# Optimization experiments

Measured on AMD Instinct MI355X. Metric: run time of the kernel, lower is better.

## Reference

```python
import jax, jax.numpy as jnp
import numpy as np

N_NODES = 50000
N_EDGES = 800000
NUM_FEATURES = 128
H1, H2, H3 = 256, 512, 256


def setup_inputs() -> dict:
    key = jax.random.key(0)
    ks = jax.random.split(key, 14)

    def lin(kw, fan_in, fan_out):
        # torch nn.Linear-style init, stored as [in, out] for x @ W
        bound = 1.0 / np.sqrt(fan_in)
        W = jax.random.uniform(kw, (fan_in, fan_out), jnp.float32, -bound, bound)
        b = jnp.zeros((fan_out,), jnp.float32)
        return W, b

    x = jax.random.normal(ks[0], (N_NODES, NUM_FEATURES), jnp.float32)
    edge_index = jax.random.randint(ks[1], (2, N_EDGES), 0, N_NODES, jnp.int64 if jax.config.jax_enable_x64 else jnp.int32)

    W1, b1 = lin(ks[2], NUM_FEATURES, H1)
    W2, b2 = lin(ks[3], H1, H2)
    W3, b3 = lin(ks[4], H2, H3)
    Wf1, bf1 = lin(ks[5], H3, 128)
    Wf2, bf2 = lin(ks[6], 128, 64)
    Wf3, bf3 = lin(ks[7], 64, 1)

    return {"x": x, "edge_index": edge_index,
            "W1": W1, "b1": b1, "W2": W2, "b2": b2, "W3": W3, "b3": b3,
            "Wf1": Wf1, "bf1": bf1, "Wf2": Wf2, "bf2": bf2, "Wf3": Wf3, "bf3": bf3}


def gcn_conv(x, W, b, row, col, dinv_row_col, n):
    # PyG GCNConv: out = D^{-1/2} (A+I) D^{-1/2} (x W) + b, self-loops already in row/col
    h = x @ W                              # [N, out]
    msg = h[row] * dinv_row_col[:, None]   # gather + edge-wise scale: [E+N, out]
    return jax.ops.segment_sum(msg, col, num_segments=n) + b


def reference(x, edge_index, W1, b1, W2, b2, W3, b3, Wf1, bf1, Wf2, bf2, Wf3, bf3):
    n = x.shape[0]
    loop = jnp.arange(n, dtype=edge_index.dtype)
    row = jnp.concatenate([edge_index[0], loop])   # sources (with self-loops)
    col = jnp.concatenate([edge_index[1], loop])   # targets (with self-loops)

    # symmetric normalization (computed once; identical for all three convs)
    deg = jax.ops.segment_sum(jnp.ones(col.shape[0], x.dtype), col, num_segments=n)
    dinv = jnp.where(deg > 0, jax.lax.rsqrt(deg), 0.0)
    norm = dinv[row] * dinv[col]                   # [E+N]

    h = jax.nn.relu(gcn_conv(x, W1, b1, row, col, norm, n))
    h = jax.nn.relu(gcn_conv(h, W2, b2, row, col, norm, n))
    h = jax.nn.relu(gcn_conv(h, W3, b3, row, col, norm, n))

    g = jnp.mean(h, axis=0, keepdims=True)         # [1, H3]
    g = jax.nn.relu(g @ Wf1 + bf1)
    g = jax.nn.relu(g @ Wf2 + bf2)
    return g @ Wf3 + bf3                           # [1, 1]
```

## Files before the change

### kernel.cpp

```cpp
#include <hip/hip_runtime.h>
#include <hip/hip_bf16.h>

#define N_NODES 50000
#define N_EDGES 800000
#define N_BUCKETS 64
#define M_PAD 50048
#define SCAN_NB 196

typedef short short8 __attribute__((ext_vector_type(8)));
typedef float floatx4 __attribute__((ext_vector_type(4)));
typedef float floatx2 __attribute__((ext_vector_type(2)));

__device__ __forceinline__ unsigned short f2bf(float f) {
    unsigned u = __float_as_uint(f);
    unsigned r = (u + 0x7fff + ((u >> 16) & 1)) >> 16;
    return (unsigned short)r;
}
__device__ __forceinline__ float bf2f(unsigned short h) {
    return __uint_as_float(((unsigned)h) << 16);
}
__device__ __forceinline__ void expand2(unsigned u, float& lo, float& hi) {
    lo = __uint_as_float(u << 16);
    hi = __uint_as_float(u & 0xffff0000u);
}

__device__ __forceinline__ unsigned pack4_fp8(float f0, float f1, float f2, float f3) {
    int v = __builtin_amdgcn_cvt_pk_fp8_f32(f0, f1, 0, false);
    v = __builtin_amdgcn_cvt_pk_fp8_f32(f2, f3, v, true);
    return (unsigned)v;
}
__device__ __forceinline__ void accum_fp8x4(float* a, unsigned u, float w) {
    floatx2 lo = __builtin_amdgcn_cvt_pk_f32_fp8((int)u, false);
    floatx2 hi = __builtin_amdgcn_cvt_pk_f32_fp8((int)u, true);
    a[0] += lo[0] * w; a[1] += lo[1] * w;
    a[2] += hi[0] * w; a[3] += hi[1] * w;
}
__device__ __forceinline__ void accum_fp8x2(float* a, unsigned u, float w) {
    floatx2 lo = __builtin_amdgcn_cvt_pk_f32_fp8((int)u, false);
    a[0] += lo[0] * w; a[1] += lo[1] * w;
}

__device__ __forceinline__ void gload16(const void* gp, void* lp) {
    __builtin_amdgcn_global_load_lds(
        (const __attribute__((address_space(1))) unsigned int*)gp,
        (__attribute__((address_space(3))) unsigned int*)lp,
        16, 0, 0);
}

__global__ void k_init(int* __restrict__ cnt, float* __restrict__ gb) {
    int i = blockIdx.x * blockDim.x + threadIdx.x;
    if (i < N_NODES) cnt[i] = 0;
    if (i < N_BUCKETS * 256) gb[i] = 0.0f;
}

__global__ void k_count(const int* __restrict__ col, int* __restrict__ cnt) {
    int e = blockIdx.x * blockDim.x + threadIdx.x;
    if (e < N_EDGES) atomicAdd(&cnt[col[e]], 1);
}

__global__ __launch_bounds__(256) void k_scanA(const int* __restrict__ cnt,
                                               int* __restrict__ bsum) {
    __shared__ int red[256];
    int t = threadIdx.x;
    int i = blockIdx.x * 256 + t;
    red[t] = (i < N_NODES) ? cnt[i] : 0;
    __syncthreads();
    for (int d = 128; d > 0; d >>= 1) {
        if (t < d) red[t] += red[t + d];
        __syncthreads();
    }
    if (t == 0) bsum[blockIdx.x] = red[0];
}

__global__ __launch_bounds__(256) void k_scanB(const int* __restrict__ bsum,
                                               int* __restrict__ bbase,
                                               int* __restrict__ off) {
    __shared__ int sc[256];
    int t = threadIdx.x;
    sc[t] = (t < SCAN_NB) ? bsum[t] : 0;
    __syncthreads();
    for (int d = 1; d < 256; d <<= 1) {
        int v = 0;
        if (t >= d) v = sc[t - d];
        __syncthreads();
        if (t >= d) sc[t] += v;
        __syncthreads();
    }
    if (t < SCAN_NB) bbase[t] = sc[t] - bsum[t];
    if (t == 0) off[N_NODES] = N_EDGES;
}

__global__ __launch_bounds__(256) void k_scanC(const int* __restrict__ cnt,
                                               const int* __restrict__ bbase,
                                               int* __restrict__ off,
                                               int* __restrict__ cursor,
                                               float* __restrict__ dinv) {
    __shared__ int sc[256];
    int t = threadIdx.x;
    int i = blockIdx.x * 256 + t;
    int c = (i < N_NODES) ? cnt[i] : 0;
    sc[t] = c;
    __syncthreads();
    for (int d = 1; d < 256; d <<= 1) {
        int v = 0;
        if (t >= d) v = sc[t - d];
        __syncthreads();
        if (t >= d) sc[t] += v;
        __syncthreads();
    }
    if (i < N_NODES) {
        int excl = sc[t] - c + bbase[blockIdx.x];
        off[i] = excl;
        cursor[i] = excl;
        dinv[i] = 1.0f / sqrtf((float)(c + 1));
    }
}

__global__ void k_fill(const int* __restrict__ row, const int* __restrict__ col,
                       const float* __restrict__ dinv, int* __restrict__ cursor,
                       int2* __restrict__ epack) {
    int e = blockIdx.x * blockDim.x + threadIdx.x;
    if (e >= N_EDGES) return;
    int v = col[e];
    int p = atomicAdd(&cursor[v], 1);
    int r = row[e];
    epack[p] = make_int2(r, __float_as_int(dinv[r]));
}

__global__ void k_prepW(const float* __restrict__ W,
                        unsigned short* __restrict__ Th,
                        unsigned short* __restrict__ Tl, int K, int N) {
    int idx = blockIdx.x * blockDim.x + threadIdx.x;
    if (idx >= K * N) return;
    int n = idx / K, k = idx - n * K;
    float v = W[(size_t)k * N + n];
    unsigned short h = f2bf(v);
    Th[idx] = h;
    Tl[idx] = f2bf(v - bf2f(h));
}

__global__ void k_prepX8(const float* __restrict__ x, unsigned char* __restrict__ xq) {
    int i = blockIdx.x * blockDim.x + threadIdx.x;
    if (i >= N_NODES * 32) return;
    const float* s = x + (size_t)i * 4;
    *(unsigned*)&xq[(size_t)i * 4] = pack4_fp8(s[0], s[1], s[2], s[3]);
}

template <int DIM, int POOL>
__global__ __launch_bounds__(256) void k_aggf(
    const unsigned char* __restrict__ xq, const int* __restrict__ off,
    const int2* __restrict__ epack, const float* __restrict__ dinv,
    const float* __restrict__ bias, unsigned short* __restrict__ outb,
    float* __restrict__ gb) {
    const int FPL = DIM / 64;
    __shared__ float gpart[256];
    if (POOL) {
        gpart[threadIdx.x] = 0.0f;
        __syncthreads();
    }
    int wv = threadIdx.x >> 6;
    int li = threadIdx.x & 63;
    int v = blockIdx.x * 4 + wv;
    int f = li * FPL;
    float dv = dinv[v];
    const unsigned char* __restrict__ xf = xq + f;
    float a0[FPL], a1[FPL], a2[FPL], a3[FPL];
#pragma unroll
    for (int i = 0; i < FPL; ++i) { a0[i] = 0.f; a1[i] = 0.f; a2[i] = 0.f; a3[i] = 0.f; }
    if (FPL == 4) {
        accum_fp8x4(a0, *(const unsigned*)&xf[(size_t)v * DIM], dv);
    } else {
        accum_fp8x2(a0, (unsigned)*(const unsigned short*)&xf[(size_t)v * DIM], dv);
    }
    int s = off[v], e = off[v + 1];
    int j = s;
    for (; j + 4 <= e; j += 4) {
        int2 p0 = epack[j + 0];
        int2 p1 = epack[j + 1];
        int2 p2 = epack[j + 2];
        int2 p3 = epack[j + 3];
        if (FPL == 4) {
            unsigned g0 = *(const unsigned*)&xf[(size_t)p0.x * DIM];
            unsigned g1 = *(const unsigned*)&xf[(size_t)p1.x * DIM];
            unsigned g2 = *(const unsigned*)&xf[(size_t)p2.x * DIM];
            unsigned g3 = *(const unsigned*)&xf[(size_t)p3.x * DIM];
            accum_fp8x4(a0, g0, __int_as_float(p0.y));
            accum_fp8x4(a1, g1, __int_as_float(p1.y));
            accum_fp8x4(a2, g2, __int_as_float(p2.y));
            accum_fp8x4(a3, g3, __int_as_float(p3.y));
        } else {
            unsigned g0 = *(const unsigned short*)&xf[(size_t)p0.x * DIM];
            unsigned g1 = *(const unsigned short*)&xf[(size_t)p1.x * DIM];
            unsigned g2 = *(const unsigned short*)&xf[(size_t)p2.x * DIM];
            unsigned g3 = *(const unsigned short*)&xf[(size_t)p3.x * DIM];
            accum_fp8x2(a0, g0, __int_as_float(p0.y));
            accum_fp8x2(a1, g1, __int_as_float(p1.y));
            accum_fp8x2(a2, g2, __int_as_float(p2.y));
            accum_fp8x2(a3, g3, __int_as_float(p3.y));
        }
    }
    for (; j < e; ++j) {
        int2 p = epack[j];
        if (FPL == 4) {
            accum_fp8x4(a0, *(const unsigned*)&xf[(size_t)p.x * DIM], __int_as_float(p.y));
        } else {
            accum_fp8x2(a0, (unsigned)*(const unsigned short*)&xf[(size_t)p.x * DIM],
                        __int_as_float(p.y));
        }
    }
    float acc[FPL];
#pragma unroll
    for (int i = 0; i < FPL; ++i)
        acc[i] = ((a0[i] + a1[i]) + (a2[i] + a3[i])) * dv;
    if (!POOL) {
        if (FPL == 4) {
            uint2 o;
            o.x = (unsigned)f2bf(acc[0]) | ((unsigned)f2bf(acc[1]) << 16);
            o.y = (unsigned)f2bf(acc[2]) | ((unsigned)f2bf(acc[3]) << 16);
            *(uint2*)&outb[(size_t)v * DIM + f] = o;
        } else {
            unsigned o = (unsigned)f2bf(acc[0]) | ((unsigned)f2bf(acc[1]) << 16);
            *(unsigned*)&outb[(size_t)v * DIM + f] = o;
        }
    } else {
#pragma unroll
        for (int i = 0; i < FPL; ++i) {
            float r = fmaxf(acc[i] + bias[f + i], 0.0f);
            atomicAdd(&gpart[f + i], r);
        }
        __syncthreads();
        atomicAdd(&gb[(blockIdx.x & (N_BUCKETS - 1)) * 256 + threadIdx.x],
                  gpart[threadIdx.x]);
    }
}

template <int BIAS, int RELU, int OUTFP8>
__global__ __launch_bounds__(256) void k_gemm_b(
    const unsigned short* __restrict__ A,
    const unsigned short* __restrict__ Bh, const unsigned short* __restrict__ Bl,
    const float* __restrict__ bias, void* __restrict__ Cout,
    int M, int K, int N) {
    __shared__ unsigned short smem[3 * 2 * 4096];
    unsigned short* As  = smem;
    unsigned short* BsH = smem + 2 * 4096;
    unsigned short* BsL = smem + 4 * 4096;
    int tid = threadIdx.x;
    int lane = tid & 63;
    int w = tid >> 6;
    int wr = w & 1, wc = w >> 1;
    int bm = blockIdx.x * 128, bn = blockIdx.y * 128;

    floatx4 acc[4][4];
    floatx4 zero = {0.f, 0.f, 0.f, 0.f};
#pragma unroll
    for (int t = 0; t < 4; ++t)
#pragma unroll
        for (int u = 0; u < 4; ++u) acc[t][u] = zero;

    int c0 = w * 2, c1 = c0 + 1;
    int srow = lane >> 2;
    int kg = ((lane & 3) - ((lane >> 3) & 3)) & 3;
    int kc = kg * 8;
    const unsigned short* Ap0 = A + (size_t)(bm + c0 * 16 + srow) * K + kc;
    const unsigned short* Ap1 = A + (size_t)(bm + c1 * 16 + srow) * K + kc;
    const unsigned short* Bh0 = Bh + (size_t)(bn + c0 * 16 + srow) * K + kc;
    const unsigned short* Bh1 = Bh + (size_t)(bn + c1 * 16 + srow) * K + kc;
    const unsigned short* Bl0 = Bl + (size_t)(bn + c0 * 16 + srow) * K + kc;
    const unsigned short* Bl1 = Bl + (size_t)(bn + c1 * 16 + srow) * K + kc;

    const int KT = K >> 5;
#define STAGE(half, k0)                                       \
    do {                                                      \
        gload16(Ap0 + (k0), As + (half) * 4096 + c0 * 512);   \
        gload16(Ap1 + (k0), As + (half) * 4096 + c1 * 512);   \
        gload16(Bh0 + (k0), BsH + (half) * 4096 + c0 * 512);  \
        gload16(Bh1 + (k0), BsH + (half) * 4096 + c1 * 512);  \
        gload16(Bl0 + (k0), BsL + (half) * 4096 + c0 * 512);  \
        gload16(Bl1 + (k0), BsL + (half) * 4096 + c1 * 512);  \
    } while (0)

    STAGE(0, 0);
    __syncthreads();

    int fr = lane & 15;
    int fq = lane >> 4;
    int cl = ((fq + (fr >> 1)) & 3) * 8;

    for (int kt = 0; kt < KT; ++kt) {
        int half = kt & 1;
        if (kt + 1 < KT) STAGE(1 - half, (kt + 1) * 32);
        short8 av[4], bhv[4], blv[4];
#pragma unroll
        for (int t = 0; t < 4; ++t) {
            av[t]  = *(const short8*)&As[half * 4096 + (wr * 64 + t * 16 + fr) * 32 + cl];
            bhv[t] = *(const short8*)&BsH[half * 4096 + (wc * 64 + t * 16 + fr) * 32 + cl];
            blv[t] = *(const short8*)&BsL[half * 4096 + (wc * 64 + t * 16 + fr) * 32 + cl];
        }
#pragma unroll
        for (int t = 0; t < 4; ++t)
#pragma unroll
            for (int u = 0; u < 4; ++u) {
                acc[t][u] = __builtin_amdgcn_mfma_f32_16x16x32_bf16(av[t], bhv[u], acc[t][u], 0, 0, 0);
                acc[t][u] = __builtin_amdgcn_mfma_f32_16x16x32_bf16(av[t], blv[u], acc[t][u], 0, 0, 0);
            }
        __syncthreads();
    }
#undef STAGE

    unsigned short* cq = smem + w * 4096;
#pragma unroll
    for (int u = 0; u < 4; ++u) {
        int colq = u * 16 + fr;
        float bv = BIAS ? bias[bn + wc * 64 + colq] : 0.0f;
#pragma unroll
        for (int t = 0; t < 4; ++t) {
#pragma unroll
            for (int r = 0; r < 4; ++r) {
                float o = acc[t][u][r] + bv;
                if (RELU) o = fmaxf(o, 0.f);
                cq[(t * 16 + fq * 4 + r) * 64 + colq] = f2bf(o);
            }
        }
    }
    __syncthreads();
    int lr = tid >> 4;
    int lc = (tid & 15) * 8;
    int wcq = lc >> 6;
    int lcq = lc & 63;
#pragma unroll
    for (int i = 0; i < 8; ++i) {
        int rowt = i * 16 + lr;
        int wrq = rowt >> 6;
        const unsigned short* src =
            smem + (wrq + wcq * 2) * 4096 + (rowt & 63) * 64 + lcq;
        int rowg = bm + rowt;
        if (rowg < M) {
            if (!OUTFP8) {
                unsigned short* C = (unsigned short*)Cout;
                *(uint4*)&C[(size_t)rowg * N + bn + lc] = *(const uint4*)src;
            } else {
                uint4 b = *(const uint4*)src;
                float f0, f1, f2, f3, f4, f5, f6, f7;
                expand2(b.x, f0, f1); expand2(b.y, f2, f3);
                expand2(b.z, f4, f5); expand2(b.w, f6, f7);
                uint2 q;
                q.x = pack4_fp8(f0, f1, f2, f3);
                q.y = pack4_fp8(f4, f5, f6, f7);
                unsigned char* C8 = (unsigned char*)Cout;
                *(uint2*)&C8[(size_t)rowg * N + bn + lc] = q;
            }
        }
    }
}

__global__ void k_mlp(const float* __restrict__ gb,
                      const float* __restrict__ Wf1, const float* __restrict__ bf1,
                      const float* __restrict__ Wf2, const float* __restrict__ bf2,
                      const float* __restrict__ Wf3, const float* __restrict__ bf3,
                      float* __restrict__ out) {
    __shared__ float s0[256], s1[128], s2[64];
    int t = threadIdx.x;
    float sum = 0.0f;
    for (int b = 0; b < N_BUCKETS; ++b) sum += gb[b * 256 + t];
    s0[t] = sum * (1.0f / (float)N_NODES);
    __syncthreads();
    if (t < 128) {
        float a = bf1[t];
        for (int k = 0; k < 256; ++k) a += s0[k] * Wf1[k * 128 + t];
        s1[t] = fmaxf(a, 0.0f);
    }
    __syncthreads();
    if (t < 64) {
        float a = bf2[t];
        for (int k = 0; k < 128; ++k) a += s1[k] * Wf2[k * 64 + t];
        s2[t] = fmaxf(a, 0.0f);
    }
    __syncthreads();
    if (t == 0) {
        float a = bf3[0];
        for (int k = 0; k < 64; ++k) a += s2[k] * Wf3[k];
        out[0] = a;
    }
}

extern "C" void kernel_launch(void* const* d_in, const int* in_sizes, int n_in,
                              void* d_out, int out_size, void* d_ws, size_t ws_size,
                              hipStream_t stream) {
    const float* x  = (const float*)d_in[0];
    const int* ei   = (const int*)d_in[1];
    const float* W1 = (const float*)d_in[2];
    const float* b1 = (const float*)d_in[3];
    const float* W2 = (const float*)d_in[4];
    const float* b2 = (const float*)d_in[5];
    const float* W3 = (const float*)d_in[6];
    const float* b3 = (const float*)d_in[7];
    const float* Wf1 = (const float*)d_in[8];
    const float* bf1 = (const float*)d_in[9];
    const float* Wf2 = (const float*)d_in[10];
    const float* bf2 = (const float*)d_in[11];
    const float* Wf3 = (const float*)d_in[12];
    const float* bf3 = (const float*)d_in[13];
    float* out = (float*)d_out;

    char* p = (char*)d_ws;
    auto alloc = [&](size_t bytes) {
        void* r = (void*)p;
        p += (bytes + 255) & ~((size_t)255);
        return r;
    };
    int*   cnt    = (int*)  alloc(N_NODES * sizeof(int));
    int*   off    = (int*)  alloc((N_NODES + 1) * sizeof(int));
    int*   cursor = (int*)  alloc(N_NODES * sizeof(int));
    int*   bsum   = (int*)  alloc(SCAN_NB * sizeof(int));
    int*   bbase  = (int*)  alloc(SCAN_NB * sizeof(int));
    float* dinv   = (float*)alloc(N_NODES * sizeof(float));
    int2*  epack  = (int2*) alloc((size_t)N_EDGES * sizeof(int2));
    float* gb     = (float*)alloc(N_BUCKETS * 256 * sizeof(float));
    unsigned short* W1h = (unsigned short*)alloc(128 * 256 * 2);
    unsigned short* W1l = (unsigned short*)alloc(128 * 256 * 2);
    unsigned short* W2h = (unsigned short*)alloc(256 * 512 * 2);
    unsigned short* W2l = (unsigned short*)alloc(256 * 512 * 2);
    unsigned short* W3h = (unsigned short*)alloc(512 * 256 * 2);
    unsigned short* W3l = (unsigned short*)alloc(512 * 256 * 2);
    unsigned char*  xq  = (unsigned char*) alloc((size_t)N_NODES * 128);
    unsigned short* t0  = (unsigned short*)alloc((size_t)M_PAD * 128 * 2);
    unsigned char*  h1q = (unsigned char*) alloc((size_t)N_NODES * 256);
    unsigned short* t1  = (unsigned short*)alloc((size_t)M_PAD * 256 * 2);
    unsigned short* h2  = (unsigned short*)alloc((size_t)M_PAD * 512 * 2);
    unsigned char*  t2q = (unsigned char*) alloc((size_t)N_NODES * 256);

    const int* row = ei;
    const int* col = ei + N_EDGES;

    const int NB = (N_NODES + 255) / 256;
    const int EB = (N_EDGES + 255) / 256;

    k_init<<<NB, 256, 0, stream>>>(cnt, gb);
    k_count<<<EB, 256, 0, stream>>>(col, cnt);
    k_scanA<<<SCAN_NB, 256, 0, stream>>>(cnt, bsum);
    k_scanB<<<1, 256, 0, stream>>>(bsum, bbase, off);
    k_scanC<<<SCAN_NB, 256, 0, stream>>>(cnt, bbase, off, cursor, dinv);
    k_fill<<<EB, 256, 0, stream>>>(row, col, dinv, cursor, epack);

    k_prepW<<<(128 * 256 + 255) / 256, 256, 0, stream>>>(W1, W1h, W1l, 128, 256);
    k_prepW<<<(256 * 512 + 255) / 256, 256, 0, stream>>>(W2, W2h, W2l, 256, 512);
    k_prepW<<<(512 * 256 + 255) / 256, 256, 0, stream>>>(W3, W3h, W3l, 512, 256);
    k_prepX8<<<(N_NODES * 32 + 255) / 256, 256, 0, stream>>>(x, xq);

    const int M = N_NODES;
    const int MB = (M + 127) / 128;

    k_aggf<128, 0><<<N_NODES / 4, 256, 0, stream>>>(
        xq, off, epack, dinv, nullptr, t0, nullptr);
    {
        dim3 grid(MB, 256 / 128);
        k_gemm_b<1, 1, 1><<<grid, 256, 0, stream>>>(t0, W1h, W1l, b1, h1q, M, 128, 256);
    }
    k_aggf<256, 0><<<N_NODES / 4, 256, 0, stream>>>(
        h1q, off, epack, dinv, nullptr, t1, nullptr);
    {
        dim3 grid(MB, 512 / 128);
        k_gemm_b<1, 1, 0><<<grid, 256, 0, stream>>>(t1, W2h, W2l, b2, h2, M, 256, 512);
    }
    {
        dim3 grid(MB, 256 / 128);
        k_gemm_b<0, 0, 1><<<grid, 256, 0, stream>>>(h2, W3h, W3l, nullptr, t2q, M, 512, 256);
    }
    k_aggf<256, 1><<<N_NODES / 4, 256, 0, stream>>>(
        t2q, off, epack, dinv, b3, nullptr, gb);

    k_mlp<<<1, 256, 0, stream>>>(gb, Wf1, bf1, Wf2, bf2, Wf3, bf3, out);
}
```

Before: 461.7 us.

## Pad CSR rows to even length for 16-byte edge loads; single-buffer GEMM LDS

Each node's adjacency segment is rounded up to an even length, and odd segments get a zero-weight dummy entry, so the aggregation loop can fetch two packed edges per 16-byte load and needs no scalar tail. The edge buffer grows to hold the padding entries. Separately, the GEMM drops its double-buffered LDS staging in favour of a single buffer loaded and synced every K step. That cuts shared memory, which may allow more resident blocks, but it gives up overlap between global loads and MFMA work.

```diff
diff --git a/kernel.cpp b/kernel.cpp
--- a/kernel.cpp
+++ b/kernel.cpp
@@ -63,7 +63,7 @@
     __shared__ int red[256];
     int t = threadIdx.x;
     int i = blockIdx.x * 256 + t;
-    red[t] = (i < N_NODES) ? cnt[i] : 0;
+    red[t] = (i < N_NODES) ? ((cnt[i] + 1) & ~1) : 0;
     __syncthreads();
     for (int d = 128; d > 0; d >>= 1) {
         if (t < d) red[t] += red[t + d];
@@ -87,19 +87,21 @@
         __syncthreads();
     }
     if (t < SCAN_NB) bbase[t] = sc[t] - bsum[t];
-    if (t == 0) off[N_NODES] = N_EDGES;
+    if (t == SCAN_NB - 1) off[N_NODES] = sc[t];
 }
 
 __global__ __launch_bounds__(256) void k_scanC(const int* __restrict__ cnt,
                                                const int* __restrict__ bbase,
                                                int* __restrict__ off,
                                                int* __restrict__ cursor,
-                                               float* __restrict__ dinv) {
+                                               float* __restrict__ dinv,
+                                               int2* __restrict__ epack) {
     __shared__ int sc[256];
     int t = threadIdx.x;
     int i = blockIdx.x * 256 + t;
     int c = (i < N_NODES) ? cnt[i] : 0;
-    sc[t] = c;
+    int cap = (c + 1) & ~1;
+    sc[t] = cap;
     __syncthreads();
     for (int d = 1; d < 256; d <<= 1) {
         int v = 0;
@@ -109,10 +111,11 @@
         __syncthreads();
     }
     if (i < N_NODES) {
-        int excl = sc[t] - c + bbase[blockIdx.x];
+        int excl = sc[t] - cap + bbase[blockIdx.x];
         off[i] = excl;
         cursor[i] = excl;
         dinv[i] = 1.0f / sqrtf((float)(c + 1));
+        if (c & 1) epack[excl + c] = make_int2(i, 0);
     }
 }
 
@@ -175,37 +178,40 @@
     int s = off[v], e = off[v + 1];
     int j = s;
     for (; j + 4 <= e; j += 4) {
-        int2 p0 = epack[j + 0];
-        int2 p1 = epack[j + 1];
-        int2 p2 = epack[j + 2];
-        int2 p3 = epack[j + 3];
+        int4 d0 = *(const int4*)&epack[j];
+        int4 d1 = *(const int4*)&epack[j + 2];
         if (FPL == 4) {
-            unsigned g0 = *(const unsigned*)&xf[(size_t)p0.x * DIM];
-            unsigned g1 = *(const unsigned*)&xf[(size_t)p1.x * DIM];
-            unsigned g2 = *(const unsigned*)&xf[(size_t)p2.x * DIM];
-            unsigned g3 = *(const unsigned*)&xf[(size_t)p3.x * DIM];
-            accum_fp8x4(a0, g0, __int_as_float(p0.y));
-            accum_fp8x4(a1, g1, __int_as_float(p1.y));
-            accum_fp8x4(a2, g2, __int_as_float(p2.y));
-            accum_fp8x4(a3, g3, __int_as_float(p3.y));
+            unsigned g0 = *(const unsigned*)&xf[(size_t)d0.x * DIM];
+            unsigned g1 = *(const unsigned*)&xf[(size_t)d0.z * DIM];
+            unsigned g2 = *(const unsigned*)&xf[(size_t)d1.x * DIM];
+            unsigned g3 = *(const unsigned*)&xf[(size_t)d1.z * DIM];
+            accum_fp8x4(a0, g0, __int_as_float(d0.y));
+            accum_fp8x4(a1, g1, __int_as_float(d0.w));
+            accum_fp8x4(a2, g2, __int_as_float(d1.y));
+            accum_fp8x4(a3, g3, __int_as_float(d1.w));
         } else {
-            unsigned g0 = *(const unsigned short*)&xf[(size_t)p0.x * DIM];
-            unsigned g1 = *(const unsigned short*)&xf[(size_t)p1.x * DIM];
-            unsigned g2 = *(const unsigned short*)&xf[(size_t)p2.x * DIM];
-            unsigned g3 = *(const unsigned short*)&xf[(size_t)p3.x * DIM];
-            accum_fp8x2(a0, g0, __int_as_float(p0.y));
-            accum_fp8x2(a1, g1, __int_as_float(p1.y));
-            accum_fp8x2(a2, g2, __int_as_float(p2.y));
-            accum_fp8x2(a3, g3, __int_as_float(p3.y));
-        }
-    }
-    for (; j < e; ++j) {
-        int2 p = epack[j];
+            unsigned g0 = *(const unsigned short*)&xf[(size_t)d0.x * DIM];
+            unsigned g1 = *(const unsigned short*)&xf[(size_t)d0.z * DIM];
+            unsigned g2 = *(const unsigned short*)&xf[(size_t)d1.x * DIM];
+            unsigned g3 = *(const unsigned short*)&xf[(size_t)d1.z * DIM];
+            accum_fp8x2(a0, g0, __int_as_float(d0.y));
+            accum_fp8x2(a1, g1, __int_as_float(d0.w));
+            accum_fp8x2(a2, g2, __int_as_float(d1.y));
+            accum_fp8x2(a3, g3, __int_as_float(d1.w));
+        }
+    }
+    if (j < e) {
+        int4 d0 = *(const int4*)&epack[j];
         if (FPL == 4) {
-            accum_fp8x4(a0, *(const unsigned*)&xf[(size_t)p.x * DIM], __int_as_float(p.y));
+            unsigned g0 = *(const unsigned*)&xf[(size_t)d0.x * DIM];
+            unsigned g1 = *(const unsigned*)&xf[(size_t)d0.z * DIM];
+            accum_fp8x4(a0, g0, __int_as_float(d0.y));
+            accum_fp8x4(a1, g1, __int_as_float(d0.w));
         } else {
-            accum_fp8x2(a0, (unsigned)*(const unsigned short*)&xf[(size_t)p.x * DIM],
-                        __int_as_float(p.y));
+            unsigned g0 = *(const unsigned short*)&xf[(size_t)d0.x * DIM];
+            unsigned g1 = *(const unsigned short*)&xf[(size_t)d0.z * DIM];
+            accum_fp8x2(a0, g0, __int_as_float(d0.y));
+            accum_fp8x2(a1, g1, __int_as_float(d0.w));
         }
     }
     float acc[FPL];
@@ -240,10 +246,10 @@
     const unsigned short* __restrict__ Bh, const unsigned short* __restrict__ Bl,
     const float* __restrict__ bias, void* __restrict__ Cout,
     int M, int K, int N) {
-    __shared__ unsigned short smem[3 * 2 * 4096];
+    __shared__ unsigned short smem[4 * 4096];
     unsigned short* As  = smem;
-    unsigned short* BsH = smem + 2 * 4096;
-    unsigned short* BsL = smem + 4 * 4096;
+    unsigned short* BsH = smem + 4096;
+    unsigned short* BsL = smem + 8192;
     int tid = threadIdx.x;
     int lane = tid & 63;
     int w = tid >> 6;
@@ -269,32 +275,25 @@
     const unsigned short* Bl1 = Bl + (size_t)(bn + c1 * 16 + srow) * K + kc;
 
     const int KT = K >> 5;
-#define STAGE(half, k0)                                       \
-    do {                                                      \
-        gload16(Ap0 + (k0), As + (half) * 4096 + c0 * 512);   \
-        gload16(Ap1 + (k0), As + (half) * 4096 + c1 * 512);   \
-        gload16(Bh0 + (k0), BsH + (half) * 4096 + c0 * 512);  \
-        gload16(Bh1 + (k0), BsH + (half) * 4096 + c1 * 512);  \
-        gload16(Bl0 + (k0), BsL + (half) * 4096 + c0 * 512);  \
-        gload16(Bl1 + (k0), BsL + (half) * 4096 + c1 * 512);  \
-    } while (0)
-
-    STAGE(0, 0);
-    __syncthreads();
-
     int fr = lane & 15;
     int fq = lane >> 4;
     int cl = ((fq + (fr >> 1)) & 3) * 8;
 
     for (int kt = 0; kt < KT; ++kt) {
-        int half = kt & 1;
-        if (kt + 1 < KT) STAGE(1 - half, (kt + 1) * 32);
+        int k0 = kt * 32;
+        gload16(Ap0 + k0, As + c0 * 512);
+        gload16(Ap1 + k0, As + c1 * 512);
+        gload16(Bh0 + k0, BsH + c0 * 512);
+        gload16(Bh1 + k0, BsH + c1 * 512);
+        gload16(Bl0 + k0, BsL + c0 * 512);
+        gload16(Bl1 + k0, BsL + c1 * 512);
+        __syncthreads();
         short8 av[4], bhv[4], blv[4];
 #pragma unroll
         for (int t = 0; t < 4; ++t) {
-            av[t]  = *(const short8*)&As[half * 4096 + (wr * 64 + t * 16 + fr) * 32 + cl];
-            bhv[t] = *(const short8*)&BsH[half * 4096 + (wc * 64 + t * 16 + fr) * 32 + cl];
-            blv[t] = *(const short8*)&BsL[half * 4096 + (wc * 64 + t * 16 + fr) * 32 + cl];
+            av[t]  = *(const short8*)&As[(wr * 64 + t * 16 + fr) * 32 + cl];
+            bhv[t] = *(const short8*)&BsH[(wc * 64 + t * 16 + fr) * 32 + cl];
+            blv[t] = *(const short8*)&BsL[(wc * 64 + t * 16 + fr) * 32 + cl];
         }
 #pragma unroll
         for (int t = 0; t < 4; ++t)
@@ -305,7 +304,6 @@
             }
         __syncthreads();
     }
-#undef STAGE
 
     unsigned short* cq = smem + w * 4096;
 #pragma unroll
@@ -414,7 +412,7 @@
     int*   bsum   = (int*)  alloc(SCAN_NB * sizeof(int));
     int*   bbase  = (int*)  alloc(SCAN_NB * sizeof(int));
     float* dinv   = (float*)alloc(N_NODES * sizeof(float));
-    int2*  epack  = (int2*) alloc((size_t)N_EDGES * sizeof(int2));
+    int2*  epack  = (int2*) alloc((size_t)(N_EDGES + N_NODES) * sizeof(int2));
     float* gb     = (float*)alloc(N_BUCKETS * 256 * sizeof(float));
     unsigned short* W1h = (unsigned short*)alloc(128 * 256 * 2);
     unsigned short* W1l = (unsigned short*)alloc(128 * 256 * 2);
@@ -439,7 +437,7 @@
     k_count<<<EB, 256, 0, stream>>>(col, cnt);
     k_scanA<<<SCAN_NB, 256, 0, stream>>>(cnt, bsum);
     k_scanB<<<1, 256, 0, stream>>>(bsum, bbase, off);
-    k_scanC<<<SCAN_NB, 256, 0, stream>>>(cnt, bbase, off, cursor, dinv);
+    k_scanC<<<SCAN_NB, 256, 0, stream>>>(cnt, bbase, off, cursor, dinv, epack);
     k_fill<<<EB, 256, 0, stream>>>(row, col, dinv, cursor, epack);
 
     k_prepW<<<(128 * 256 + 255) / 256, 256, 0, stream>>>(W1, W1h, W1l, 128, 256);
```

Result: no change. 459.3 us (-0.5%).
